# Kernel tuning notes

Hardware: AMD Instinct MI355X
Metric: run time of the kernel (lower is better)

## Reference

```python
import jax, jax.numpy as jnp
import numpy as np

B, T, H = 32, 2048, 512


def setup_inputs() -> dict:
    key = jax.random.key(0)
    ks = jax.random.split(key, 6)
    s = 1.0 / np.sqrt(T)  # keep tanh/softmax in a sane range (glorot-ish)
    return {
        "x": jax.random.normal(ks[0], (B, T, H), dtype=jnp.float32),
        "t": jax.random.normal(ks[1], (B, T, H), dtype=jnp.float32),
        "kernel_x": jax.random.normal(ks[2], (T, T), dtype=jnp.float32) * s,
        "kernel_t": jax.random.normal(ks[3], (T, T), dtype=jnp.float32) * s,
        "kernel_a": jax.random.normal(ks[4], (T, T), dtype=jnp.float32) * s,
        "bias_x": jnp.zeros((T,), dtype=jnp.float32),
        "bias_t": jnp.zeros((T,), dtype=jnp.float32),
        "lambd": jax.random.uniform(ks[5], (H, 1), dtype=jnp.float32),
    }


def reference(x, t, kernel_x, kernel_t, kernel_a, bias_x, bias_t, lambd):
    # Permute (2,1): [B, T, H] -> [B, H, T]
    xp = jnp.swapaxes(x, 1, 2)
    tp = jnp.swapaxes(t, 1, 2)
    # gamma/beta: [B, H, T] @ [T, T] + bias, then tanh
    gamma = jnp.tanh(jnp.einsum('bht,ts->bhs', xp, kernel_x) + bias_x)
    beta = jnp.tanh(jnp.einsum('bht,ts->bhs', tp, kernel_t) + bias_t)
    # Convex combination with learned lambd [H, 1] broadcasting over T
    delta = lambd * gamma + (1.0 - lambd) * beta
    # Attention weights: softmax over last (timestamp) axis
    alpha = jax.nn.softmax(jnp.einsum('bht,ts->bhs', delta, kernel_a), axis=-1)
    # Permute back: [B, H, T] -> [B, T, H]
    return jnp.swapaxes(alpha, 1, 2)
```

## Files before the change

### kernel.cpp

```cpp
#include <hip/hip_runtime.h>

constexpr int Bc = 32, Tc = 2048, Hc = 512;

typedef _Float16 f16;
typedef _Float16 f16x8 __attribute__((ext_vector_type(8)));
typedef float f32x4 __attribute__((ext_vector_type(4)));

__device__ __forceinline__ void gload_lds16(const void* g, void* l) {
  __builtin_amdgcn_global_load_lds(
      (const __attribute__((address_space(1))) void*)g,
      (__attribute__((address_space(3))) void*)l, 16, 0, 0);
}

__device__ __forceinline__ float fast_exp(float x) {
  return __builtin_amdgcn_exp2f(x * 1.4426950408889634f);
}
__device__ __forceinline__ float fast_tanh(float x) {
  const float z = __builtin_amdgcn_exp2f(x * 2.8853900817779268f);
  return (z - 1.0f) * __builtin_amdgcn_rcpf(z + 1.0f);
}

__global__ __launch_bounds__(256) void cvt_bth(const float* __restrict__ xin,
                                               const float* __restrict__ tin,
                                               f16* __restrict__ xo,
                                               f16* __restrict__ to) {
  __shared__ f16 tile[64][65];
  const int tid = threadIdx.x;
  const int c = tid & 63, r0 = tid >> 6;
  const int t0 = blockIdx.x * 64, h0 = blockIdx.y * 64;
  int z = blockIdx.z;
  const float* src;
  f16* dst;
  if (z < Bc) { src = xin; dst = xo; } else { src = tin; dst = to; z -= Bc; }
  src += (size_t)z * Tc * Hc;
  dst += (size_t)z * Hc * Tc;
#pragma unroll
  for (int rr = 0; rr < 64; rr += 4)
    tile[rr + r0][c] = (f16)src[(size_t)(t0 + rr + r0) * Hc + h0 + c];
  __syncthreads();
#pragma unroll
  for (int rr = 0; rr < 64; rr += 4)
    dst[(size_t)(h0 + rr + r0) * Tc + t0 + c] = tile[c][rr + r0];
}

__global__ __launch_bounds__(256) void cvt_tt(const float* __restrict__ kx,
                                              const float* __restrict__ kt,
                                              const float* __restrict__ ka,
                                              f16* __restrict__ ox,
                                              f16* __restrict__ ot,
                                              f16* __restrict__ oa) {
  __shared__ f16 tile[64][65];
  const int tid = threadIdx.x;
  const int c = tid & 63, r0 = tid >> 6;
  const int t0 = blockIdx.x * 64, s0 = blockIdx.y * 64;
  const float* src = blockIdx.z == 0 ? kx : (blockIdx.z == 1 ? kt : ka);
  f16* dst = blockIdx.z == 0 ? ox : (blockIdx.z == 1 ? ot : oa);
#pragma unroll
  for (int rr = 0; rr < 64; rr += 4)
    tile[rr + r0][c] = (f16)src[(size_t)(t0 + rr + r0) * Tc + s0 + c];
  __syncthreads();
#pragma unroll
  for (int rr = 0; rr < 64; rr += 4)
    dst[(size_t)(s0 + rr + r0) * Tc + t0 + c] = tile[c][rr + r0];
}

template <int MODE>
__global__ __launch_bounds__(512, 2) void gemm_k(const f16* __restrict__ A,
                                                 const f16* __restrict__ Bm,
                                                 void* __restrict__ Cout,
                                                 const f16* __restrict__ Gprev,
                                                 const float* __restrict__ bias,
                                                 const float* __restrict__ lambd,
                                                 float* __restrict__ psums) {
  extern __shared__ char smem[];
  constexpr int BK = 32, NT = Tc / BK;
  constexpr int ABYTES = 256 * BK * 2;
  const int tid = threadIdx.x;
  const int lane = tid & 63, w = tid >> 6;
  const int wr = w >> 2, wc = w & 3;
  const int l15 = lane & 15, kg = lane >> 4;

  int id = (int)blockIdx.x;
  id = (id & 7) * ((int)gridDim.x >> 3) + (id >> 3);
  int b, m0, n0;
  if constexpr (MODE == 2) {
    b = id >> 4; m0 = ((id >> 1) & 7) * 256; n0 = (id & 1) * 256;
  } else {
    b = 0; m0 = (id >> 3) * 256; n0 = (id & 7) * 256;
  }

  const size_t K = Tc;
  const size_t HT = (size_t)Hc * Tc;
  const f16* Ag = A + (size_t)m0 * K;
  const f16* Bg = Bm + (MODE == 2 ? (size_t)b * HT : (size_t)0) + (size_t)n0 * K;

  const int r4 = lane >> 2;
  const int cswz = ((lane & 3) ^ ((lane >> 3) & 3)) * 8;
  const int sr0 = (w * 2 + 0) * 16 + r4, sr1 = (w * 2 + 1) * 16 + r4;
  const f16* gA0 = Ag + (size_t)sr0 * K + cswz;
  const f16* gA1 = Ag + (size_t)sr1 * K + cswz;
  const f16* gB0 = Bg + (size_t)sr0 * K + cswz;
  const f16* gB1 = Bg + (size_t)sr1 * K + cswz;
  char* lA = smem;
  char* lB = smem + 4 * ABYTES;
  const int lo0 = (w * 2 + 0) * 1024, lo1 = (w * 2 + 1) * 1024;

  const int xk = (kg ^ ((l15 >> 1) & 3)) * 16;
  const int aoff = (wr * 128 + l15) * 64 + xk;
  const int boff = (wc * 64 + l15) * 64 + xk;

  f32x4 acc[8][4];
#pragma unroll
  for (int i = 0; i < 8; ++i)
#pragma unroll
    for (int j = 0; j < 4; ++j) acc[i][j] = {0.f, 0.f, 0.f, 0.f};

#pragma unroll
  for (int p = 0; p < 3; ++p) {
    char* dA = lA + p * ABYTES;
    char* dB = lB + p * ABYTES;
    gload_lds16(gA0 + (size_t)p * BK, dA + lo0);
    gload_lds16(gA1 + (size_t)p * BK, dA + lo1);
    gload_lds16(gB0 + (size_t)p * BK, dB + lo0);
    gload_lds16(gB1 + (size_t)p * BK, dB + lo1);
  }
  asm volatile("s_waitcnt vmcnt(8)");
  __builtin_amdgcn_s_barrier();
  __builtin_amdgcn_sched_barrier(0);

  for (int t = 0; t < NT; ++t) {
    char* curA = lA + (t & 3) * ABYTES;
    char* curB = lB + (t & 3) * ABYTES;
    const int tn = t + 3;
    char* nA = lA + (tn & 3) * ABYTES;
    char* nB = lB + (tn & 3) * ABYTES;

    f16x8 bf[4], af[4], ag[4];
#pragma unroll
    for (int j = 0; j < 4; ++j) bf[j] = *(const f16x8*)(curB + boff + j * 1024);
#pragma unroll
    for (int i = 0; i < 4; ++i) af[i] = *(const f16x8*)(curA + aoff + i * 1024);
#pragma unroll
    for (int i = 0; i < 4; ++i) ag[i] = *(const f16x8*)(curA + aoff + (4 + i) * 1024);
    __builtin_amdgcn_sched_barrier(0);

    if (tn < NT) {
      gload_lds16(gA0 + (size_t)tn * BK, nA + lo0);
      gload_lds16(gA1 + (size_t)tn * BK, nA + lo1);
      gload_lds16(gB0 + (size_t)tn * BK, nB + lo0);
      gload_lds16(gB1 + (size_t)tn * BK, nB + lo1);
    }
    asm volatile("s_waitcnt lgkmcnt(0)");
    __builtin_amdgcn_s_setprio(1);
#pragma unroll
    for (int i = 0; i < 4; ++i)
#pragma unroll
      for (int j = 0; j < 4; ++j)
        acc[i][j] = __builtin_amdgcn_mfma_f32_16x16x32_f16(af[i], bf[j], acc[i][j], 0, 0, 0);
    __builtin_amdgcn_s_setprio(0);

    if (t < NT - 3) {
      asm volatile("s_waitcnt vmcnt(8)");
    } else if (t == NT - 3) {
      asm volatile("s_waitcnt vmcnt(4)");
    } else {
      asm volatile("s_waitcnt vmcnt(0)");
    }
    __builtin_amdgcn_s_barrier();
    __builtin_amdgcn_sched_barrier(0);

    __builtin_amdgcn_s_setprio(1);
#pragma unroll
    for (int i = 0; i < 4; ++i)
#pragma unroll
      for (int j = 0; j < 4; ++j)
        acc[4 + i][j] = __builtin_amdgcn_mfma_f32_16x16x32_f16(ag[i], bf[j], acc[4 + i][j], 0, 0, 0);
    __builtin_amdgcn_s_setprio(0);
  }

  float psum[4] = {0.f, 0.f, 0.f, 0.f};
#pragma unroll
  for (int i = 0; i < 8; ++i) {
#pragma unroll
    for (int r = 0; r < 4; ++r) {
      const int gr = m0 + wr * 128 + i * 16 + kg * 4 + r;
#pragma unroll
      for (int j = 0; j < 4; ++j) {
        const int gc = n0 + wc * 64 + j * 16 + l15;
        const float v = acc[i][j][r];
        if constexpr (MODE == 0) {
          f16* C = (f16*)Cout;
          C[(size_t)gr * Tc + gc] = (f16)fast_tanh(v + bias[gc]);
        } else if constexpr (MODE == 1) {
          f16* C = (f16*)Cout;
          const size_t idx = (size_t)gr * Tc + gc;
          const float g = (float)Gprev[idx];
          const float lam = lambd[gr & 511];
          C[idx] = (f16)(lam * g + (1.f - lam) * fast_tanh(v + bias[gc]));
        } else {
          f16* Es = (f16*)Cout;
          const float e = fast_exp(v);
          Es[((size_t)b * Tc + gr) * Hc + gc] = (f16)e;
          psum[j] += e;
        }
      }
    }
  }
  if constexpr (MODE == 2) {
    float* ps = (float*)smem;
    __syncthreads();
#pragma unroll
    for (int j = 0; j < 4; ++j)
      ps[(wr * 4 + kg) * 256 + (wc * 64 + j * 16 + l15)] = psum[j];
    __syncthreads();
    if (tid < 256) {
      float s = 0.f;
#pragma unroll
      for (int p = 0; p < 8; ++p) s += ps[p * 256 + tid];
      psums[((size_t)b * 8 + (m0 >> 8)) * Hc + n0 + tid] = s;
    }
  }
}

__global__ __launch_bounds__(1024) void norm_k(const f16* __restrict__ Es,
                                               const float* __restrict__ psums,
                                               float* __restrict__ out) {
  __shared__ float inv[512];
  const int tid = threadIdx.x;
  const int b = blockIdx.x >> 3, sseg = blockIdx.x & 7;
  if (tid < 512) {
    float s = 0.f;
    const float* P = psums + (size_t)b * 8 * Hc + tid;
#pragma unroll
    for (int p = 0; p < 8; ++p) s += P[p * Hc];
    inv[tid] = 1.f / s;
  }
  __syncthreads();
  const int hg = (tid & 63) * 8;
  const int so = tid >> 6;
  float iv[8];
#pragma unroll
  for (int j = 0; j < 8; ++j) iv[j] = inv[hg + j];
  const size_t base = ((size_t)b * Tc + sseg * 256) * Hc;
  for (int r = so; r < 256; r += 16) {
    const size_t idx = base + (size_t)r * Hc + hg;
    const f16x8 e = *(const f16x8*)(Es + idx);
    float4 o0, o1;
    o0.x = (float)e[0] * iv[0]; o0.y = (float)e[1] * iv[1];
    o0.z = (float)e[2] * iv[2]; o0.w = (float)e[3] * iv[3];
    o1.x = (float)e[4] * iv[4]; o1.y = (float)e[5] * iv[5];
    o1.z = (float)e[6] * iv[6]; o1.w = (float)e[7] * iv[7];
    *(float4*)(out + idx) = o0;
    *(float4*)(out + idx + 4) = o1;
  }
}

extern "C" void kernel_launch(void* const* d_in, const int* in_sizes, int n_in,
                              void* d_out, int out_size, void* d_ws, size_t ws_size,
                              hipStream_t stream) {
  const float* x  = (const float*)d_in[0];
  const float* tt = (const float*)d_in[1];
  const float* kx = (const float*)d_in[2];
  const float* kt = (const float*)d_in[3];
  const float* ka = (const float*)d_in[4];
  const float* bx = (const float*)d_in[5];
  const float* bt = (const float*)d_in[6];
  const float* lm = (const float*)d_in[7];
  float* out = (float*)d_out;

  const size_t NBHT = (size_t)Bc * Hc * Tc;

  f16* XhT = (f16*)d_out;
  f16* ThT = XhT + NBHT;

  f16* Gt  = (f16*)d_ws;
  f16* Dt  = Gt + NBHT;
  f16* KxT = Dt + NBHT;
  f16* KtT = KxT + (size_t)Tc * Tc;
  f16* KaT = KtT + (size_t)Tc * Tc;
  float* Ps = (float*)KxT;
  f16* Es = Gt;

  constexpr int LDS_BYTES = 8 * 256 * 32 * 2;
  (void)hipFuncSetAttribute(reinterpret_cast<const void*>(gemm_k<0>),
                            hipFuncAttributeMaxDynamicSharedMemorySize, LDS_BYTES);
  (void)hipFuncSetAttribute(reinterpret_cast<const void*>(gemm_k<1>),
                            hipFuncAttributeMaxDynamicSharedMemorySize, LDS_BYTES);
  (void)hipFuncSetAttribute(reinterpret_cast<const void*>(gemm_k<2>),
                            hipFuncAttributeMaxDynamicSharedMemorySize, LDS_BYTES);

  cvt_bth<<<dim3(Tc / 64, Hc / 64, Bc * 2), 256, 0, stream>>>(x, tt, XhT, ThT);
  cvt_tt<<<dim3(Tc / 64, Tc / 64, 3), 256, 0, stream>>>(kx, kt, ka, KxT, KtT, KaT);
  gemm_k<0><<<512, 512, LDS_BYTES, stream>>>(XhT, KxT, Gt, nullptr, bx, nullptr, nullptr);
  gemm_k<1><<<512, 512, LDS_BYTES, stream>>>(ThT, KtT, Dt, Gt, bt, lm, nullptr);
  gemm_k<2><<<512, 512, LDS_BYTES, stream>>>(KaT, Dt, Es, nullptr, nullptr, nullptr, Ps);
  norm_k<<<dim3(Bc * 8), 1024, 0, stream>>>(Es, Ps, out);
}
```

Baseline: 536.5 us.

## Software-pipeline LDS fragment reads across K-iterations with double-buffered registers

```diff
diff --git a/kernel.cpp b/kernel.cpp
--- a/kernel.cpp
+++ b/kernel.cpp
@@ -124,58 +124,102 @@
     gload_lds16(gB0 + (size_t)p * BK, dB + lo0);
     gload_lds16(gB1 + (size_t)p * BK, dB + lo1);
   }
-  asm volatile("s_waitcnt vmcnt(8)");
+  asm volatile("s_waitcnt vmcnt(4)");
   __builtin_amdgcn_s_barrier();
   __builtin_amdgcn_sched_barrier(0);
 
-  for (int t = 0; t < NT; ++t) {
-    char* curA = lA + (t & 3) * ABYTES;
-    char* curB = lB + (t & 3) * ABYTES;
-    const int tn = t + 3;
-    char* nA = lA + (tn & 3) * ABYTES;
-    char* nB = lB + (tn & 3) * ABYTES;
-
-    f16x8 bf[4], af[4], ag[4];
-#pragma unroll
-    for (int j = 0; j < 4; ++j) bf[j] = *(const f16x8*)(curB + boff + j * 1024);
-#pragma unroll
-    for (int i = 0; i < 4; ++i) af[i] = *(const f16x8*)(curA + aoff + i * 1024);
-#pragma unroll
-    for (int i = 0; i < 4; ++i) ag[i] = *(const f16x8*)(curA + aoff + (4 + i) * 1024);
-    __builtin_amdgcn_sched_barrier(0);
-
-    if (tn < NT) {
-      gload_lds16(gA0 + (size_t)tn * BK, nA + lo0);
-      gload_lds16(gA1 + (size_t)tn * BK, nA + lo1);
-      gload_lds16(gB0 + (size_t)tn * BK, nB + lo0);
-      gload_lds16(gB1 + (size_t)tn * BK, nB + lo1);
+  f16x8 afP[4], bfP[4], afN[4], bfN[4], ag[4];
+#pragma unroll
+  for (int j = 0; j < 4; ++j) bfP[j] = *(const f16x8*)(lB + boff + j * 1024);
+#pragma unroll
+  for (int i = 0; i < 4; ++i) afP[i] = *(const f16x8*)(lA + aoff + i * 1024);
+
+  for (int t = 0; t < NT; t += 2) {
+    {
+      char* curA = lA + (t & 3) * ABYTES;
+      char* nxtA = lA + ((t + 1) & 3) * ABYTES;
+      char* nxtB = lB + ((t + 1) & 3) * ABYTES;
+#pragma unroll
+      for (int i = 0; i < 4; ++i) ag[i] = *(const f16x8*)(curA + aoff + (4 + i) * 1024);
+      if (t + 3 < NT) {
+        char* sA = lA + ((t + 3) & 3) * ABYTES;
+        char* sB = lB + ((t + 3) & 3) * ABYTES;
+        gload_lds16(gA0 + (size_t)(t + 3) * BK, sA + lo0);
+        gload_lds16(gA1 + (size_t)(t + 3) * BK, sA + lo1);
+        gload_lds16(gB0 + (size_t)(t + 3) * BK, sB + lo0);
+        gload_lds16(gB1 + (size_t)(t + 3) * BK, sB + lo1);
+      }
+      if (t < NT - 4) {
+        asm volatile("s_waitcnt vmcnt(4)");
+      } else {
+        asm volatile("s_waitcnt vmcnt(0)");
+      }
+      __builtin_amdgcn_s_setprio(1);
+#pragma unroll
+      for (int i = 0; i < 4; ++i)
+#pragma unroll
+        for (int j = 0; j < 4; ++j)
+          acc[i][j] = __builtin_amdgcn_mfma_f32_16x16x32_f16(afP[i], bfP[j], acc[i][j], 0, 0, 0);
+      __builtin_amdgcn_s_setprio(0);
+#pragma unroll
+      for (int j = 0; j < 4; ++j) bfN[j] = *(const f16x8*)(nxtB + boff + j * 1024);
+#pragma unroll
+      for (int i = 0; i < 4; ++i) afN[i] = *(const f16x8*)(nxtA + aoff + i * 1024);
+      __builtin_amdgcn_s_setprio(1);
+#pragma unroll
+      for (int i = 0; i < 4; ++i)
+#pragma unroll
+        for (int j = 0; j < 4; ++j)
+          acc[4 + i][j] = __builtin_amdgcn_mfma_f32_16x16x32_f16(ag[i], bfP[j], acc[4 + i][j], 0, 0, 0);
+      __builtin_amdgcn_s_setprio(0);
+      __builtin_amdgcn_sched_barrier(0);
+      __builtin_amdgcn_s_barrier();
+      __builtin_amdgcn_sched_barrier(0);
     }
-    asm volatile("s_waitcnt lgkmcnt(0)");
-    __builtin_amdgcn_s_setprio(1);
-#pragma unroll
-    for (int i = 0; i < 4; ++i)
-#pragma unroll
-      for (int j = 0; j < 4; ++j)
-        acc[i][j] = __builtin_amdgcn_mfma_f32_16x16x32_f16(af[i], bf[j], acc[i][j], 0, 0, 0);
-    __builtin_amdgcn_s_setprio(0);
-
-    if (t < NT - 3) {
-      asm volatile("s_waitcnt vmcnt(8)");
-    } else if (t == NT - 3) {
-      asm volatile("s_waitcnt vmcnt(4)");
-    } else {
-      asm volatile("s_waitcnt vmcnt(0)");
+    {
+      const int u = t + 1;
+      char* curA = lA + (u & 3) * ABYTES;
+      char* nx2A = lA + ((u + 1) & 3) * ABYTES;
+      char* nx2B = lB + ((u + 1) & 3) * ABYTES;
+#pragma unroll
+      for (int i = 0; i < 4; ++i) ag[i] = *(const f16x8*)(curA + aoff + (4 + i) * 1024);
+      if (u + 3 < NT) {
+        char* sA = lA + ((u + 3) & 3) * ABYTES;
+        char* sB = lB + ((u + 3) & 3) * ABYTES;
+        gload_lds16(gA0 + (size_t)(u + 3) * BK, sA + lo0);
+        gload_lds16(gA1 + (size_t)(u + 3) * BK, sA + lo1);
+        gload_lds16(gB0 + (size_t)(u + 3) * BK, sB + lo0);
+        gload_lds16(gB1 + (size_t)(u + 3) * BK, sB + lo1);
+      }
+      if (u < NT - 4) {
+        asm volatile("s_waitcnt vmcnt(4)");
+      } else {
+        asm volatile("s_waitcnt vmcnt(0)");
+      }
+      __builtin_amdgcn_s_setprio(1);
+#pragma unroll
+      for (int i = 0; i < 4; ++i)
+#pragma unroll
+        for (int j = 0; j < 4; ++j)
+          acc[i][j] = __builtin_amdgcn_mfma_f32_16x16x32_f16(afN[i], bfN[j], acc[i][j], 0, 0, 0);
+      __builtin_amdgcn_s_setprio(0);
+      if (u + 1 < NT) {
+#pragma unroll
+        for (int j = 0; j < 4; ++j) bfP[j] = *(const f16x8*)(nx2B + boff + j * 1024);
+#pragma unroll
+        for (int i = 0; i < 4; ++i) afP[i] = *(const f16x8*)(nx2A + aoff + i * 1024);
+      }
+      __builtin_amdgcn_s_setprio(1);
+#pragma unroll
+      for (int i = 0; i < 4; ++i)
+#pragma unroll
+        for (int j = 0; j < 4; ++j)
+          acc[4 + i][j] = __builtin_amdgcn_mfma_f32_16x16x32_f16(ag[i], bfN[j], acc[4 + i][j], 0, 0, 0);
+      __builtin_amdgcn_s_setprio(0);
+      __builtin_amdgcn_sched_barrier(0);
+      __builtin_amdgcn_s_barrier();
+      __builtin_amdgcn_sched_barrier(0);
     }
-    __builtin_amdgcn_s_barrier();
-    __builtin_amdgcn_sched_barrier(0);
-
-    __builtin_amdgcn_s_setprio(1);
-#pragma unroll
-    for (int i = 0; i < 4; ++i)
-#pragma unroll
-      for (int j = 0; j < 4; ++j)
-        acc[4 + i][j] = __builtin_amdgcn_mfma_f32_16x16x32_f16(ag[i], bf[j], acc[4 + i][j], 0, 0, 0);
-    __builtin_amdgcn_s_setprio(0);
   }
 
   float psum[4] = {0.f, 0.f, 0.f, 0.f};
```

Result: no change. 533.5 us (-0.6%).

## Shrink GEMM tile to 128x256 with 4 waves, triple-buffer, vectorize transposes

Applied to the files above, without the earlier changes.

```diff
diff --git a/kernel.cpp b/kernel.cpp
--- a/kernel.cpp
+++ b/kernel.cpp
@@ -26,7 +26,6 @@
                                                f16* __restrict__ to) {
   __shared__ f16 tile[64][65];
   const int tid = threadIdx.x;
-  const int c = tid & 63, r0 = tid >> 6;
   const int t0 = blockIdx.x * 64, h0 = blockIdx.y * 64;
   int z = blockIdx.z;
   const float* src;
@@ -34,13 +33,25 @@
   if (z < Bc) { src = xin; dst = xo; } else { src = tin; dst = to; z -= Bc; }
   src += (size_t)z * Tc * Hc;
   dst += (size_t)z * Hc * Tc;
-#pragma unroll
-  for (int rr = 0; rr < 64; rr += 4)
-    tile[rr + r0][c] = (f16)src[(size_t)(t0 + rr + r0) * Hc + h0 + c];
+  const int c4 = tid & 15, r0 = tid >> 4;
+#pragma unroll
+  for (int rr = 0; rr < 64; rr += 16) {
+    const float4 v = *(const float4*)(src + (size_t)(t0 + rr + r0) * Hc + h0 + c4 * 4);
+    tile[rr + r0][c4 * 4 + 0] = (f16)v.x;
+    tile[rr + r0][c4 * 4 + 1] = (f16)v.y;
+    tile[rr + r0][c4 * 4 + 2] = (f16)v.z;
+    tile[rr + r0][c4 * 4 + 3] = (f16)v.w;
+  }
   __syncthreads();
-#pragma unroll
-  for (int rr = 0; rr < 64; rr += 4)
-    dst[(size_t)(h0 + rr + r0) * Tc + t0 + c] = tile[c][rr + r0];
+  const int tc = tid & 7, hr = tid >> 3;
+#pragma unroll
+  for (int hp = 0; hp < 64; hp += 32) {
+    const int h = hp + hr;
+    f16x8 o;
+#pragma unroll
+    for (int j = 0; j < 8; ++j) o[j] = tile[tc * 8 + j][h];
+    *(f16x8*)(dst + (size_t)(h0 + h) * Tc + t0 + tc * 8) = o;
+  }
 }
 
 __global__ __launch_bounds__(256) void cvt_tt(const float* __restrict__ kx,
@@ -51,21 +62,32 @@
                                               f16* __restrict__ oa) {
   __shared__ f16 tile[64][65];
   const int tid = threadIdx.x;
-  const int c = tid & 63, r0 = tid >> 6;
   const int t0 = blockIdx.x * 64, s0 = blockIdx.y * 64;
   const float* src = blockIdx.z == 0 ? kx : (blockIdx.z == 1 ? kt : ka);
   f16* dst = blockIdx.z == 0 ? ox : (blockIdx.z == 1 ? ot : oa);
-#pragma unroll
-  for (int rr = 0; rr < 64; rr += 4)
-    tile[rr + r0][c] = (f16)src[(size_t)(t0 + rr + r0) * Tc + s0 + c];
+  const int c4 = tid & 15, r0 = tid >> 4;
+#pragma unroll
+  for (int rr = 0; rr < 64; rr += 16) {
+    const float4 v = *(const float4*)(src + (size_t)(t0 + rr + r0) * Tc + s0 + c4 * 4);
+    tile[rr + r0][c4 * 4 + 0] = (f16)v.x;
+    tile[rr + r0][c4 * 4 + 1] = (f16)v.y;
+    tile[rr + r0][c4 * 4 + 2] = (f16)v.z;
+    tile[rr + r0][c4 * 4 + 3] = (f16)v.w;
+  }
   __syncthreads();
-#pragma unroll
-  for (int rr = 0; rr < 64; rr += 4)
-    dst[(size_t)(s0 + rr + r0) * Tc + t0 + c] = tile[c][rr + r0];
+  const int tc = tid & 7, sr = tid >> 3;
+#pragma unroll
+  for (int sp = 0; sp < 64; sp += 32) {
+    const int s = sp + sr;
+    f16x8 o;
+#pragma unroll
+    for (int j = 0; j < 8; ++j) o[j] = tile[tc * 8 + j][s];
+    *(f16x8*)(dst + (size_t)(s0 + s) * Tc + t0 + tc * 8) = o;
+  }
 }
 
 template <int MODE>
-__global__ __launch_bounds__(512, 2) void gemm_k(const f16* __restrict__ A,
+__global__ __launch_bounds__(256, 2) void gemm_k(const f16* __restrict__ A,
                                                  const f16* __restrict__ Bm,
                                                  void* __restrict__ Cout,
                                                  const f16* __restrict__ Gprev,
@@ -74,19 +96,19 @@
                                                  float* __restrict__ psums) {
   extern __shared__ char smem[];
   constexpr int BK = 32, NT = Tc / BK;
-  constexpr int ABYTES = 256 * BK * 2;
+  constexpr int BUFB = 24576;
   const int tid = threadIdx.x;
   const int lane = tid & 63, w = tid >> 6;
-  const int wr = w >> 2, wc = w & 3;
+  const int wr = w >> 1, wc = w & 1;
   const int l15 = lane & 15, kg = lane >> 4;
 
   int id = (int)blockIdx.x;
   id = (id & 7) * ((int)gridDim.x >> 3) + (id >> 3);
   int b, m0, n0;
   if constexpr (MODE == 2) {
-    b = id >> 4; m0 = ((id >> 1) & 7) * 256; n0 = (id & 1) * 256;
+    b = id >> 5; m0 = ((id >> 1) & 15) * 128; n0 = (id & 1) * 256;
   } else {
-    b = 0; m0 = (id >> 3) * 256; n0 = (id & 7) * 256;
+    b = 0; m0 = (id >> 3) * 128; n0 = (id & 7) * 256;
   }
 
   const size_t K = Tc;
@@ -96,73 +118,62 @@
 
   const int r4 = lane >> 2;
   const int cswz = ((lane & 3) ^ ((lane >> 3) & 3)) * 8;
-  const int sr0 = (w * 2 + 0) * 16 + r4, sr1 = (w * 2 + 1) * 16 + r4;
-  const f16* gA0 = Ag + (size_t)sr0 * K + cswz;
-  const f16* gA1 = Ag + (size_t)sr1 * K + cswz;
-  const f16* gB0 = Bg + (size_t)sr0 * K + cswz;
-  const f16* gB1 = Bg + (size_t)sr1 * K + cswz;
-  char* lA = smem;
-  char* lB = smem + 4 * ABYTES;
-  const int lo0 = (w * 2 + 0) * 1024, lo1 = (w * 2 + 1) * 1024;
+  const f16* gA0 = Ag + (size_t)(w * 32 + r4) * K + cswz;
+  const f16* gA1 = gA0 + (size_t)16 * K;
+  const f16* gB0 = Bg + (size_t)(w * 64 + r4) * K + cswz;
+  const f16* gB1 = gB0 + (size_t)16 * K;
+  const f16* gB2 = gB0 + (size_t)32 * K;
+  const f16* gB3 = gB0 + (size_t)48 * K;
+  const int sA0 = w * 2048, sA1 = sA0 + 1024;
+  const int sB0 = 8192 + w * 4096;
 
   const int xk = (kg ^ ((l15 >> 1) & 3)) * 16;
-  const int aoff = (wr * 128 + l15) * 64 + xk;
-  const int boff = (wc * 64 + l15) * 64 + xk;
-
-  f32x4 acc[8][4];
-#pragma unroll
-  for (int i = 0; i < 8; ++i)
-#pragma unroll
-    for (int j = 0; j < 4; ++j) acc[i][j] = {0.f, 0.f, 0.f, 0.f};
-
-#pragma unroll
-  for (int p = 0; p < 3; ++p) {
-    char* dA = lA + p * ABYTES;
-    char* dB = lB + p * ABYTES;
-    gload_lds16(gA0 + (size_t)p * BK, dA + lo0);
-    gload_lds16(gA1 + (size_t)p * BK, dA + lo1);
-    gload_lds16(gB0 + (size_t)p * BK, dB + lo0);
-    gload_lds16(gB1 + (size_t)p * BK, dB + lo1);
-  }
-  asm volatile("s_waitcnt vmcnt(8)");
+  const int aoff = (wr * 64 + l15) * 64 + xk;
+  const int boff = 8192 + (wc * 128 + l15) * 64 + xk;
+
+  f32x4 acc[4][8];
+#pragma unroll
+  for (int i = 0; i < 4; ++i)
+#pragma unroll
+    for (int j = 0; j < 8; ++j) acc[i][j] = {0.f, 0.f, 0.f, 0.f};
+
+#define STAGE6(ktile, buf) do {                                        \
+    char* dd = smem + (buf) * BUFB;                                    \
+    gload_lds16(gA0 + (size_t)(ktile) * BK, dd + sA0);                 \
+    gload_lds16(gA1 + (size_t)(ktile) * BK, dd + sA1);                 \
+    gload_lds16(gB0 + (size_t)(ktile) * BK, dd + sB0);                 \
+    gload_lds16(gB1 + (size_t)(ktile) * BK, dd + sB0 + 1024);          \
+    gload_lds16(gB2 + (size_t)(ktile) * BK, dd + sB0 + 2048);          \
+    gload_lds16(gB3 + (size_t)(ktile) * BK, dd + sB0 + 3072); } while (0)
+
+  STAGE6(0, 0);
+  STAGE6(1, 1);
+  asm volatile("s_waitcnt vmcnt(6)");
   __builtin_amdgcn_s_barrier();
   __builtin_amdgcn_sched_barrier(0);
 
   for (int t = 0; t < NT; ++t) {
-    char* curA = lA + (t & 3) * ABYTES;
-    char* curB = lB + (t & 3) * ABYTES;
-    const int tn = t + 3;
-    char* nA = lA + (tn & 3) * ABYTES;
-    char* nB = lB + (tn & 3) * ABYTES;
-
-    f16x8 bf[4], af[4], ag[4];
-#pragma unroll
-    for (int j = 0; j < 4; ++j) bf[j] = *(const f16x8*)(curB + boff + j * 1024);
-#pragma unroll
-    for (int i = 0; i < 4; ++i) af[i] = *(const f16x8*)(curA + aoff + i * 1024);
-#pragma unroll
-    for (int i = 0; i < 4; ++i) ag[i] = *(const f16x8*)(curA + aoff + (4 + i) * 1024);
+    char* cur = smem + (t % 3) * BUFB;
+
+    f16x8 af[4], bf[8];
+#pragma unroll
+    for (int j = 0; j < 8; ++j) bf[j] = *(const f16x8*)(cur + boff + j * 1024);
+#pragma unroll
+    for (int i = 0; i < 4; ++i) af[i] = *(const f16x8*)(cur + aoff + i * 1024);
     __builtin_amdgcn_sched_barrier(0);
 
-    if (tn < NT) {
-      gload_lds16(gA0 + (size_t)tn * BK, nA + lo0);
-      gload_lds16(gA1 + (size_t)tn * BK, nA + lo1);
-      gload_lds16(gB0 + (size_t)tn * BK, nB + lo0);
-      gload_lds16(gB1 + (size_t)tn * BK, nB + lo1);
-    }
+    if (t + 2 < NT) STAGE6(t + 2, (t + 2) % 3);
     asm volatile("s_waitcnt lgkmcnt(0)");
     __builtin_amdgcn_s_setprio(1);
 #pragma unroll
-    for (int i = 0; i < 4; ++i)
-#pragma unroll
-      for (int j = 0; j < 4; ++j)
+    for (int i = 0; i < 2; ++i)
+#pragma unroll
+      for (int j = 0; j < 8; ++j)
         acc[i][j] = __builtin_amdgcn_mfma_f32_16x16x32_f16(af[i], bf[j], acc[i][j], 0, 0, 0);
     __builtin_amdgcn_s_setprio(0);
 
-    if (t < NT - 3) {
-      asm volatile("s_waitcnt vmcnt(8)");
-    } else if (t == NT - 3) {
-      asm volatile("s_waitcnt vmcnt(4)");
+    if (t < NT - 2) {
+      asm volatile("s_waitcnt vmcnt(6)");
     } else {
       asm volatile("s_waitcnt vmcnt(0)");
     }
@@ -171,22 +182,25 @@
 
     __builtin_amdgcn_s_setprio(1);
 #pragma unroll
-    for (int i = 0; i < 4; ++i)
-#pragma unroll
-      for (int j = 0; j < 4; ++j)
-        acc[4 + i][j] = __builtin_amdgcn_mfma_f32_16x16x32_f16(ag[i], bf[j], acc[4 + i][j], 0, 0, 0);
+    for (int i = 2; i < 4; ++i)
+#pragma unroll
+      for (int j = 0; j < 8; ++j)
+        acc[i][j] = __builtin_amdgcn_mfma_f32_16x16x32_f16(af[i], bf[j], acc[i][j], 0, 0, 0);
     __builtin_amdgcn_s_setprio(0);
   }
-
-  float psum[4] = {0.f, 0.f, 0.f, 0.f};
-#pragma unroll
-  for (int i = 0; i < 8; ++i) {
+#undef STAGE6
+
+  float psum[8];
+#pragma unroll
+  for (int j = 0; j < 8; ++j) psum[j] = 0.f;
+#pragma unroll
+  for (int i = 0; i < 4; ++i) {
 #pragma unroll
     for (int r = 0; r < 4; ++r) {
-      const int gr = m0 + wr * 128 + i * 16 + kg * 4 + r;
-#pragma unroll
-      for (int j = 0; j < 4; ++j) {
-        const int gc = n0 + wc * 64 + j * 16 + l15;
+      const int gr = m0 + wr * 64 + i * 16 + kg * 4 + r;
+#pragma unroll
+      for (int j = 0; j < 8; ++j) {
+        const int gc = n0 + wc * 128 + j * 16 + l15;
         const float v = acc[i][j][r];
         if constexpr (MODE == 0) {
           f16* C = (f16*)Cout;
@@ -209,15 +223,16 @@
   if constexpr (MODE == 2) {
     float* ps = (float*)smem;
     __syncthreads();
-#pragma unroll
-    for (int j = 0; j < 4; ++j)
-      ps[(wr * 4 + kg) * 256 + (wc * 64 + j * 16 + l15)] = psum[j];
+    const int part = wr * 4 + kg;
+#pragma unroll
+    for (int j = 0; j < 8; ++j)
+      ps[part * 256 + wc * 128 + j * 16 + l15] = psum[j];
     __syncthreads();
-    if (tid < 256) {
+    {
       float s = 0.f;
 #pragma unroll
       for (int p = 0; p < 8; ++p) s += ps[p * 256 + tid];
-      psums[((size_t)b * 8 + (m0 >> 8)) * Hc + n0 + tid] = s;
+      psums[((size_t)b * 16 + (m0 >> 7)) * Hc + n0 + tid] = s;
     }
   }
 }
@@ -227,12 +242,12 @@
                                                float* __restrict__ out) {
   __shared__ float inv[512];
   const int tid = threadIdx.x;
-  const int b = blockIdx.x >> 3, sseg = blockIdx.x & 7;
+  const int b = blockIdx.x >> 4, sseg = blockIdx.x & 15;
   if (tid < 512) {
     float s = 0.f;
-    const float* P = psums + (size_t)b * 8 * Hc + tid;
-#pragma unroll
-    for (int p = 0; p < 8; ++p) s += P[p * Hc];
+    const float* P = psums + (size_t)b * 16 * Hc + tid;
+#pragma unroll
+    for (int p = 0; p < 16; ++p) s += P[p * Hc];
     inv[tid] = 1.f / s;
   }
   __syncthreads();
@@ -241,8 +256,8 @@
   float iv[8];
 #pragma unroll
   for (int j = 0; j < 8; ++j) iv[j] = inv[hg + j];
-  const size_t base = ((size_t)b * Tc + sseg * 256) * Hc;
-  for (int r = so; r < 256; r += 16) {
+  const size_t base = ((size_t)b * Tc + sseg * 128) * Hc;
+  for (int r = so; r < 128; r += 16) {
     const size_t idx = base + (size_t)r * Hc + hg;
     const f16x8 e = *(const f16x8*)(Es + idx);
     float4 o0, o1;
@@ -281,7 +296,7 @@
   float* Ps = (float*)KxT;
   f16* Es = Gt;
 
-  constexpr int LDS_BYTES = 8 * 256 * 32 * 2;
+  constexpr int LDS_BYTES = 3 * 24576;
   (void)hipFuncSetAttribute(reinterpret_cast<const void*>(gemm_k<0>),
                             hipFuncAttributeMaxDynamicSharedMemorySize, LDS_BYTES);
   (void)hipFuncSetAttribute(reinterpret_cast<const void*>(gemm_k<1>),
@@ -291,8 +306,8 @@
 
   cvt_bth<<<dim3(Tc / 64, Hc / 64, Bc * 2), 256, 0, stream>>>(x, tt, XhT, ThT);
   cvt_tt<<<dim3(Tc / 64, Tc / 64, 3), 256, 0, stream>>>(kx, kt, ka, KxT, KtT, KaT);
-  gemm_k<0><<<512, 512, LDS_BYTES, stream>>>(XhT, KxT, Gt, nullptr, bx, nullptr, nullptr);
-  gemm_k<1><<<512, 512, LDS_BYTES, stream>>>(ThT, KtT, Dt, Gt, bt, lm, nullptr);
-  gemm_k<2><<<512, 512, LDS_BYTES, stream>>>(KaT, Dt, Es, nullptr, nullptr, nullptr, Ps);
-  norm_k<<<dim3(Bc * 8), 1024, 0, stream>>>(Es, Ps, out);
-}
+  gemm_k<0><<<1024, 256, LDS_BYTES, stream>>>(XhT, KxT, Gt, nullptr, bx, nullptr, nullptr);
+  gemm_k<1><<<1024, 256, LDS_BYTES, stream>>>(ThT, KtT, Dt, Gt, bt, lm, nullptr);
+  gemm_k<2><<<1024, 256, LDS_BYTES, stream>>>(KaT, Dt, Es, nullptr, nullptr, nullptr, Ps);
+  norm_k<<<dim3(Bc * 16), 1024, 0, stream>>>(Es, Ps, out);
+}
```

After: 573.6 us. 6.9% more time.
